# Performance work log

Measured on AMD Instinct MI355X. Metric: run time of the kernel, lower is better.

The kernel has to match this reference:

```python
import jax, jax.numpy as jnp
import numpy as np

N = 50000      # total atoms in batched graph
E = 800000     # edges
IN = 128       # in_feats
OUT = 64       # out_feats (per GAT head)
H = 4          # num_heads
NEG_SLOPE = 0.2
BN_EPS = 1e-5


def setup_inputs() -> dict:
    key = jax.random.key(0)
    ks = jax.random.split(key, 16)
    s = 0.1  # keep activations well-scaled
    return {
        "node_feats": jax.random.normal(ks[0], (N, IN), jnp.float32),
        "W_fc":       jax.random.normal(ks[1], (IN, H * OUT), jnp.float32) * s,
        "attn_l":     jax.random.normal(ks[2], (H, OUT), jnp.float32) * s,
        "attn_r":     jax.random.normal(ks[3], (H, OUT), jnp.float32) * s,
        "gat_res_w":  jax.random.normal(ks[4], (IN, H * OUT), jnp.float32) * s,
        "gat_bias":   jax.random.normal(ks[5], (H * OUT,), jnp.float32) * s,
        "conv_w":     jax.random.normal(ks[6], (1, H, 1), jnp.float32) * s,
        "conv_b":     jax.random.normal(ks[7], (1,), jnp.float32) * s,
        "res_w":      jax.random.normal(ks[8], (IN, OUT), jnp.float32) * s,
        "res_b":      jax.random.normal(ks[9], (OUT,), jnp.float32) * s,
        "bn_gamma":   jnp.ones((OUT,), jnp.float32),
        "bn_beta":    jnp.zeros((OUT,), jnp.float32),
        "src":        jax.random.randint(ks[10], (E,), 0, N, jnp.int32),
        "dst":        jax.random.randint(ks[11], (E,), 0, N, jnp.int32),
        "etype":      0,
    }


def reference(node_feats, W_fc, attn_l, attn_r, gat_res_w, gat_bias,
              conv_w, conv_b, res_w, res_b, bn_gamma, bn_beta,
              src, dst, etype):
    # ---- GATConv (DGL semantics, eval mode: no dropout) ----
    h = (node_feats @ W_fc).reshape(-1, H, OUT)            # [N,H,D]
    el = jnp.sum(h * attn_l, axis=-1)                      # [N,H]
    er = jnp.sum(h * attn_r, axis=-1)                      # [N,H]
    e = jax.nn.leaky_relu(el[src] + er[dst], NEG_SLOPE)    # [E,H]
    # segment softmax over incoming edges of each dst node
    m = jax.ops.segment_max(e, dst, num_segments=N)        # [N,H]
    m = jnp.where(jnp.isfinite(m), m, 0.0)                 # empty segments
    a = jnp.exp(e - m[dst])                                # [E,H]
    ssum = jax.ops.segment_sum(a, dst, num_segments=N)     # [N,H]
    alpha = a / (ssum[dst] + 1e-16)                        # [E,H]
    # weighted aggregation: rst[v] = sum_{(u->v)} alpha * h[u]
    rst = jax.ops.segment_sum(alpha[:, :, None] * h[src], dst, num_segments=N)  # [N,H,D]
    # GAT residual (in != H*OUT -> linear res_fc, no bias) + bias + activation
    rst = rst + (node_feats @ gat_res_w).reshape(-1, H, OUT) + gat_bias.reshape(H, OUT)
    rst = jax.nn.relu(rst)                                 # [N,H,D]
    # ---- Conv1d(4 -> 1, kernel=1): weighted head merge ----
    y = jnp.einsum("nhd,h->nd", rst, conv_w[0, :, 0]) + conv_b[0]  # [N,D]
    # ---- outer residual ----
    y = y + jax.nn.relu(node_feats @ res_w + res_b)
    # ---- BatchNorm1d (training-style batch stats) ----
    mean = jnp.mean(y, axis=0)
    var = jnp.var(y, axis=0)
    return (y - mean) / jnp.sqrt(var + BN_EPS) * bn_gamma + bn_beta
```

## Files before the change

### kernel.cpp

```cpp
#include <hip/hip_runtime.h>

#define IN_F   128
#define OUTD   64
#define HOUT   256
#define RESTC  320
#define NEG_SLOPE 0.2f
#define BN_EPS 1e-5f
#define HIST_BLOCKS 512
#define BPAD 136

typedef __attribute__((ext_vector_type(8))) short bf16x8;
typedef __attribute__((ext_vector_type(4))) float f32x4;
typedef __attribute__((ext_vector_type(2))) float f32x2;

__device__ __forceinline__ unsigned short f2bf(float f) {
    union { float f; unsigned u; } v; v.f = f;
    unsigned r = (v.u + 0x7FFF + ((v.u >> 16) & 1)) >> 16;
    return (unsigned short)r;
}
__device__ __forceinline__ float bf2f(unsigned short h) {
    union { unsigned u; float f; } v; v.u = ((unsigned)h) << 16;
    return v.f;
}

__global__ __launch_bounds__(256) void k0_pack(
    const float* __restrict__ W_fc, const float* __restrict__ W_gres,
    const float* __restrict__ W_res, unsigned short* __restrict__ Btg)
{
    int idx = blockIdx.x * 256 + threadIdx.x;
    if (idx >= 576 * 128) return;
    int c = idx >> 7, k = idx & 127;
    float v;
    if (c < 256)      v = W_fc[k * HOUT + c];
    else if (c < 512) v = W_gres[k * HOUT + (c - 256)];
    else              v = W_res[k * OUTD + (c - 512)];
    Btg[idx] = f2bf(v);
}

__global__ __launch_bounds__(256) void k1_gemm(
    const float* __restrict__ A, const unsigned short* __restrict__ Btg,
    const float* __restrict__ attn_l, const float* __restrict__ attn_r,
    const int* __restrict__ dst, int* __restrict__ degree, int* __restrict__ rank,
    unsigned char* __restrict__ Hh8, unsigned short* __restrict__ Hrest,
    float* __restrict__ el, float* __restrict__ er,
    int N, int E, int Mtiles)
{
    __shared__ __align__(16) unsigned short As[128 * BPAD];
    __shared__ __align__(16) unsigned short Bs[64 * BPAD];
    int bid = blockIdx.x, t = threadIdx.x;

    if (bid >= Mtiles) {
        int hb = bid - Mtiles;
        for (int e = hb * 256 + t; e < E; e += HIST_BLOCKS * 256)
            rank[e] = atomicAdd(degree + dst[e], 1);
        return;
    }

    int m0 = bid * 128;

    for (int i = 0; i < 16; ++i) {
        int slot = t + i * 256;
        int r = slot >> 5, c4 = (slot & 31) << 2;
        float4 v = make_float4(0.f, 0.f, 0.f, 0.f);
        if (m0 + r < N) v = *(const float4*)(A + (size_t)(m0 + r) * IN_F + c4);
        ushort4 o;
        o.x = f2bf(v.x); o.y = f2bf(v.y); o.z = f2bf(v.z); o.w = f2bf(v.w);
        *(ushort4*)(&As[r * BPAD + c4]) = o;
    }

    int w = t >> 6, lane = t & 63, quad = lane >> 4, n15 = lane & 15;
    bf16x8 af[2][4];
    unsigned hpack[2][4][4] = {};

    for (int n = 0; n < 9; ++n) {
        if (n) __syncthreads();
        for (int i = 0; i < 4; ++i) {
            int slot = t + i * 256;
            int c = slot >> 4, k0 = (slot & 15) << 3;
            *(uint4*)(&Bs[c * BPAD + k0]) = *(const uint4*)(Btg + (size_t)(n * 64 + c) * IN_F + k0);
        }
        __syncthreads();
        if (n == 0) {
#pragma unroll
            for (int i = 0; i < 2; ++i)
#pragma unroll
                for (int ks = 0; ks < 4; ++ks)
                    af[i][ks] = *(const bf16x8*)(&As[(w * 32 + i * 16 + n15) * BPAD + ks * 32 + quad * 8]);
        }

        f32x4 acc[2][4] = {};
#pragma unroll
        for (int ks = 0; ks < 4; ++ks) {
            bf16x8 bfr[4];
#pragma unroll
            for (int j = 0; j < 4; ++j)
                bfr[j] = *(const bf16x8*)(&Bs[(j * 16 + n15) * BPAD + ks * 32 + quad * 8]);
#pragma unroll
            for (int i = 0; i < 2; ++i)
#pragma unroll
                for (int j = 0; j < 4; ++j)
                    acc[i][j] = __builtin_amdgcn_mfma_f32_16x16x32_bf16(af[i][ks], bfr[j], acc[i][j], 0, 0, 0);
        }

        if (n < 4) {
            float alv[4], arv[4];
#pragma unroll
            for (int j = 0; j < 4; ++j) {
                alv[j] = attn_l[n * 64 + j * 16 + n15];
                arv[j] = attn_r[n * 64 + j * 16 + n15];
            }
#pragma unroll
            for (int i = 0; i < 2; ++i)
#pragma unroll
                for (int reg = 0; reg < 4; ++reg) {
                    float pl = acc[i][0][reg] * alv[0] + acc[i][1][reg] * alv[1]
                             + acc[i][2][reg] * alv[2] + acc[i][3][reg] * alv[3];
                    float pr = acc[i][0][reg] * arv[0] + acc[i][1][reg] * arv[1]
                             + acc[i][2][reg] * arv[2] + acc[i][3][reg] * arv[3];
#pragma unroll
                    for (int off = 1; off < 16; off <<= 1) {
                        pl += __shfl_xor(pl, off);
                        pr += __shfl_xor(pr, off);
                    }
                    int r = m0 + w * 32 + i * 16 + quad * 4 + reg;
                    if (n15 == 0 && r < N) {
                        el[(size_t)r * 4 + n] = pl;
                        er[(size_t)r * 4 + n] = pr;
                    }
                }
#pragma unroll
            for (int i = 0; i < 2; ++i)
#pragma unroll
                for (int j = 0; j < 4; ++j)
#pragma unroll
                    for (int reg = 0; reg < 4; ++reg) {
                        float v = acc[i][j][reg];
                        unsigned pk = (unsigned)__builtin_amdgcn_cvt_pk_fp8_f32(v, v, 0, false);
                        hpack[i][j][reg] |= (pk & 0xffu) << (8 * n);
                    }
        } else {
            int c0 = (n - 4) * 64;
#pragma unroll
            for (int i = 0; i < 2; ++i) {
                int rbase = m0 + w * 32 + i * 16 + quad * 4;
#pragma unroll
                for (int reg = 0; reg < 4; ++reg) {
                    int r = rbase + reg;
                    if (r < N) {
#pragma unroll
                        for (int j = 0; j < 4; ++j)
                            Hrest[(size_t)r * RESTC + c0 + j * 16 + n15] = f2bf(acc[i][j][reg]);
                    }
                }
            }
        }
    }

#pragma unroll
    for (int i = 0; i < 2; ++i) {
        int rbase = m0 + w * 32 + i * 16 + quad * 4;
#pragma unroll
        for (int reg = 0; reg < 4; ++reg) {
            int r = rbase + reg;
            if (r < N) {
#pragma unroll
                for (int j = 0; j < 4; ++j)
                    *(unsigned*)(Hh8 + (size_t)r * 256 + (j * 16 + n15) * 4) = hpack[i][j][reg];
            }
        }
    }
}

__global__ __launch_bounds__(256) void scanA_kernel(const int* __restrict__ degree,
                                                    int* __restrict__ excl,
                                                    int* __restrict__ blocksum, int N) {
    __shared__ int sm[256];
    int t = threadIdx.x;
    int i = blockIdx.x * 256 + t;
    int d = (i < N) ? degree[i] : 0;
    sm[t] = d; __syncthreads();
    for (int off = 1; off < 256; off <<= 1) {
        int v = (t >= off) ? sm[t - off] : 0;
        __syncthreads();
        sm[t] += v;
        __syncthreads();
    }
    if (i < N) excl[i] = sm[t] - d;
    if (t == 255) blocksum[blockIdx.x] = sm[255];
}

__global__ __launch_bounds__(256) void scanB_kernel(const int* __restrict__ blocksum,
                                                    int* __restrict__ base, int nb) {
    __shared__ int sm[256];
    int t = threadIdx.x;
    int d = (t < nb) ? blocksum[t] : 0;
    sm[t] = d; __syncthreads();
    for (int off = 1; off < 256; off <<= 1) {
        int v = (t >= off) ? sm[t - off] : 0;
        __syncthreads();
        sm[t] += v;
        __syncthreads();
    }
    if (t < nb) base[t] = sm[t] - d;
}

__global__ void scatter_kernel(const int* __restrict__ src, const int* __restrict__ dst,
                               const int* __restrict__ rank, const int* __restrict__ excl,
                               const int* __restrict__ base,
                               const float* __restrict__ el, const float* __restrict__ er,
                               uint4* __restrict__ es_sorted, int E) {
    int e = blockIdx.x * 256 + threadIdx.x;
    if (e >= E) return;
    int d = dst[e], u = src[e];
    int p = excl[d] + base[d >> 8] + rank[e];
    float4 l = *(const float4*)(el + (size_t)u * 4);
    float4 r = *(const float4*)(er + (size_t)d * 4);
    float x, s0, s1, s2, s3;
    x = l.x + r.x; x = x > 0.f ? x : NEG_SLOPE * x; s0 = __expf(x);
    x = l.y + r.y; x = x > 0.f ? x : NEG_SLOPE * x; s1 = __expf(x);
    x = l.z + r.z; x = x > 0.f ? x : NEG_SLOPE * x; s2 = __expf(x);
    x = l.w + r.w; x = x > 0.f ? x : NEG_SLOPE * x; s3 = __expf(x);
    uint4 o;
    o.x = (unsigned)u;
    o.y = (unsigned)f2bf(s0) | ((unsigned)f2bf(s1) << 16);
    o.z = (unsigned)f2bf(s2) | ((unsigned)f2bf(s3) << 16);
    o.w = 0u;
    es_sorted[p] = o;
}

__global__ __launch_bounds__(256) void agg_kernel(
    const unsigned char* __restrict__ Hh8, const unsigned short* __restrict__ Hrest,
    const int* __restrict__ excl, const int* __restrict__ base,
    const uint4* __restrict__ es_sorted,
    const float* __restrict__ gat_bias, const float* __restrict__ conv_w,
    const float* __restrict__ conv_b, const float* __restrict__ res_b,
    float* __restrict__ y, int N, int E)
{
    int wave = threadIdx.x >> 6, lane = threadIdx.x & 63;
    int v = blockIdx.x * 4 + wave;
    if (v >= N) return;
    int b  = excl[v] + base[v >> 8];
    int e2 = (v + 1 < N) ? (excl[v + 1] + base[(v + 1) >> 8]) : E;
    int deg = e2 - b;

    float a0 = 0.f, a1 = 0.f, a2 = 0.f, a3 = 0.f;
    float p0 = 0.f, p1 = 0.f, p2 = 0.f, p3 = 0.f;

    for (int i0 = 0; i0 < deg; i0 += 64) {
        int j = i0 + lane;
        uint4 es = make_uint4(0u, 0u, 0u, 0u);
        if (j < deg) es = es_sorted[b + j];
        p0 += bf2f((unsigned short)(es.y & 0xffff));
        p1 += bf2f((unsigned short)(es.y >> 16));
        p2 += bf2f((unsigned short)(es.z & 0xffff));
        p3 += bf2f((unsigned short)(es.z >> 16));
        int cl = deg - i0; if (cl > 64) cl = 64;
        for (int jj = 0; jj < cl; ++jj) {
            unsigned uu  = __shfl(es.x, jj);
            unsigned s01 = __shfl(es.y, jj);
            unsigned s23 = __shfl(es.z, jj);
            unsigned hv = *(const unsigned*)(Hh8 + (size_t)uu * 256 + lane * 4);
            f32x2 lo = __builtin_amdgcn_cvt_pk_f32_fp8(hv, false);
            f32x2 hi = __builtin_amdgcn_cvt_pk_f32_fp8(hv, true);
            a0 += bf2f((unsigned short)(s01 & 0xffff)) * lo.x;
            a1 += bf2f((unsigned short)(s01 >> 16))    * lo.y;
            a2 += bf2f((unsigned short)(s23 & 0xffff)) * hi.x;
            a3 += bf2f((unsigned short)(s23 >> 16))    * hi.y;
        }
    }
#pragma unroll
    for (int off = 1; off < 64; off <<= 1) {
        p0 += __shfl_xor(p0, off); p1 += __shfl_xor(p1, off);
        p2 += __shfl_xor(p2, off); p3 += __shfl_xor(p3, off);
    }
    float r0 = 1.f / (p0 + 1e-16f), r1 = 1.f / (p1 + 1e-16f);
    float r2 = 1.f / (p2 + 1e-16f), r3 = 1.f / (p3 + 1e-16f);

    const unsigned short* hr = Hrest + (size_t)v * RESTC;
    float yv = conv_b[0];
    float tt;
    tt = a0 * r0 + bf2f(hr[lane])       + gat_bias[lane];       tt = tt > 0.f ? tt : 0.f; yv += conv_w[0] * tt;
    tt = a1 * r1 + bf2f(hr[64 + lane])  + gat_bias[64 + lane];  tt = tt > 0.f ? tt : 0.f; yv += conv_w[1] * tt;
    tt = a2 * r2 + bf2f(hr[128 + lane]) + gat_bias[128 + lane]; tt = tt > 0.f ? tt : 0.f; yv += conv_w[2] * tt;
    tt = a3 * r3 + bf2f(hr[192 + lane]) + gat_bias[192 + lane]; tt = tt > 0.f ? tt : 0.f; yv += conv_w[3] * tt;
    float resv = bf2f(hr[256 + lane]) + res_b[lane];
    yv += resv > 0.f ? resv : 0.f;
    y[(size_t)v * OUTD + lane] = yv;
}

__global__ __launch_bounds__(256) void bn_partial_kernel(const float* __restrict__ y,
                                                         float* __restrict__ bnsum,
                                                         float* __restrict__ bnsumsq, int total) {
    __shared__ float smem[256];
    int t = threadIdx.x;
    size_t idx = (size_t)blockIdx.x * 256 + t;
    size_t stride = (size_t)gridDim.x * 256;
    float sum = 0.f, sq = 0.f;
    for (; idx < (size_t)total; idx += stride) {
        float v = y[idx];
        sum += v; sq += v * v;
    }
    int d = t & 63;
    smem[t] = sum; __syncthreads();
    if (t < 64) atomicAdd(bnsum + d, smem[t] + smem[t + 64] + smem[t + 128] + smem[t + 192]);
    __syncthreads();
    smem[t] = sq; __syncthreads();
    if (t < 64) atomicAdd(bnsumsq + d, smem[t] + smem[t + 64] + smem[t + 128] + smem[t + 192]);
}

__global__ void norm_kernel(const float* __restrict__ y,
                            const float* __restrict__ bnsum, const float* __restrict__ bnsumsq,
                            const float* __restrict__ gamma, const float* __restrict__ beta,
                            float* __restrict__ out, int total4, float invN) {
    int idx = blockIdx.x * blockDim.x + threadIdx.x;
    if (idx >= total4) return;
    float4 v = *(const float4*)(y + (size_t)idx * 4);
    int d = (idx * 4) & 63;
    float4 o;
#pragma unroll
    for (int k = 0; k < 4; ++k) {
        float mean = bnsum[d + k] * invN;
        float var = bnsumsq[d + k] * invN - mean * mean;
        float sc = gamma[d + k] * rsqrtf(var + BN_EPS);
        float sh = beta[d + k] - mean * sc;
        float val = (&v.x)[k] * sc + sh;
        (&o.x)[k] = val;
    }
    *(float4*)(out + (size_t)idx * 4) = o;
}

extern "C" void kernel_launch(void* const* d_in, const int* in_sizes, int n_in,
                              void* d_out, int out_size, void* d_ws, size_t ws_size,
                              hipStream_t stream) {
    const float* node_feats = (const float*)d_in[0];
    const float* W_fc       = (const float*)d_in[1];
    const float* attn_l     = (const float*)d_in[2];
    const float* attn_r     = (const float*)d_in[3];
    const float* gat_res_w  = (const float*)d_in[4];
    const float* gat_bias   = (const float*)d_in[5];
    const float* conv_w     = (const float*)d_in[6];
    const float* conv_b     = (const float*)d_in[7];
    const float* res_w      = (const float*)d_in[8];
    const float* res_b      = (const float*)d_in[9];
    const float* bn_gamma   = (const float*)d_in[10];
    const float* bn_beta    = (const float*)d_in[11];
    const int*   src        = (const int*)d_in[12];
    const int*   dst        = (const int*)d_in[13];

    const int N = in_sizes[0] / IN_F;
    const int E = in_sizes[12];
    const int Mtiles = (N + 127) / 128;
    const int nb = (N + 255) / 256;

    char* ws = (char*)d_ws;
    size_t off = 0;
    auto alloc = [&](size_t bytes) -> void* {
        void* p = (void*)(ws + off);
        off += (bytes + 255) & ~(size_t)255;
        return p;
    };

    int*   degree  = (int*)alloc((size_t)N * 4);
    float* bnsum   = (float*)alloc(64 * 4);
    float* bnsumsq = (float*)alloc(64 * 4);
    size_t zero_bytes = off;
    int*            rank      = (int*)alloc((size_t)E * 4);
    int*            excl      = (int*)alloc((size_t)N * 4);
    int*            blocksum  = (int*)alloc(256 * 4);
    int*            base      = (int*)alloc(256 * 4);
    uint4*          es_sorted = (uint4*)alloc((size_t)E * 16);
    unsigned short* Btg       = (unsigned short*)alloc((size_t)576 * IN_F * 2);
    unsigned char*  Hh8       = (unsigned char*)alloc((size_t)N * 256);
    unsigned short* Hrest     = (unsigned short*)alloc((size_t)N * RESTC * 2);
    float*          el        = (float*)alloc((size_t)N * 4 * 4);
    float*          er        = (float*)alloc((size_t)N * 4 * 4);
    float*          y         = (float*)alloc((size_t)N * OUTD * 4);
    (void)ws_size; (void)n_in; (void)out_size;

    hipMemsetAsync(d_ws, 0, zero_bytes, stream);

    k0_pack<<<(576 * 128 + 255) / 256, 256, 0, stream>>>(W_fc, gat_res_w, res_w, Btg);
    k1_gemm<<<Mtiles + HIST_BLOCKS, 256, 0, stream>>>(node_feats, Btg, attn_l, attn_r,
                                                      dst, degree, rank, Hh8, Hrest,
                                                      el, er, N, E, Mtiles);
    scanA_kernel<<<nb, 256, 0, stream>>>(degree, excl, blocksum, N);
    scanB_kernel<<<1, 256, 0, stream>>>(blocksum, base, nb);
    scatter_kernel<<<(E + 255) / 256, 256, 0, stream>>>(src, dst, rank, excl, base,
                                                        el, er, es_sorted, E);
    agg_kernel<<<(N + 3) / 4, 256, 0, stream>>>(Hh8, Hrest, excl, base, es_sorted,
                                                gat_bias, conv_w, conv_b, res_b, y, N, E);
    bn_partial_kernel<<<512, 256, 0, stream>>>(y, bnsum, bnsumsq, N * OUTD);
    norm_kernel<<<(N * OUTD / 4 + 255) / 256, 256, 0, stream>>>(y, bnsum, bnsumsq,
                                                                bn_gamma, bn_beta, (float*)d_out,
                                                                N * OUTD / 4, 1.f / (float)N);
}
```

Measured before the change: 268.5 us.

## Store GAT residual in fp8 with folded biases, shrink GEMM tile, unroll aggregation

The GAT residual projection is now written as interleaved fp8 (Hr8) with gat_bias folded in, and the outer residual as bf16 with res_b folded in. This replaces the wide bf16 Hrest buffer, cutting GEMM write traffic and agg read traffic. The GEMM M-tile drops from 128 to 64 rows, giving more blocks and lower register use. The agg inner loop uses readlane with a 2-way unroll and a pre-shifted source offset. fp8 residuals add quantization error.

```diff
diff --git a/kernel.cpp b/kernel.cpp
--- a/kernel.cpp
+++ b/kernel.cpp
@@ -3,7 +3,6 @@
 #define IN_F   128
 #define OUTD   64
 #define HOUT   256
-#define RESTC  320
 #define NEG_SLOPE 0.2f
 #define BN_EPS 1e-5f
 #define HIST_BLOCKS 512
@@ -40,12 +39,14 @@
 __global__ __launch_bounds__(256) void k1_gemm(
     const float* __restrict__ A, const unsigned short* __restrict__ Btg,
     const float* __restrict__ attn_l, const float* __restrict__ attn_r,
+    const float* __restrict__ gat_bias, const float* __restrict__ res_b,
     const int* __restrict__ dst, int* __restrict__ degree, int* __restrict__ rank,
-    unsigned char* __restrict__ Hh8, unsigned short* __restrict__ Hrest,
+    unsigned char* __restrict__ Hh8, unsigned char* __restrict__ Hr8,
+    unsigned short* __restrict__ Rres,
     float* __restrict__ el, float* __restrict__ er,
     int N, int E, int Mtiles)
 {
-    __shared__ __align__(16) unsigned short As[128 * BPAD];
+    __shared__ __align__(16) unsigned short As[64 * BPAD];
     __shared__ __align__(16) unsigned short Bs[64 * BPAD];
     int bid = blockIdx.x, t = threadIdx.x;
 
@@ -56,9 +57,9 @@
         return;
     }
 
-    int m0 = bid * 128;
-
-    for (int i = 0; i < 16; ++i) {
+    int m0 = bid * 64;
+
+    for (int i = 0; i < 8; ++i) {
         int slot = t + i * 256;
         int r = slot >> 5, c4 = (slot & 31) << 2;
         float4 v = make_float4(0.f, 0.f, 0.f, 0.f);
@@ -69,8 +70,9 @@
     }
 
     int w = t >> 6, lane = t & 63, quad = lane >> 4, n15 = lane & 15;
-    bf16x8 af[2][4];
-    unsigned hpack[2][4][4] = {};
+    bf16x8 af[4];
+    unsigned hpack[4][4] = {};
+    unsigned rpack[4][4] = {};
 
     for (int n = 0; n < 9; ++n) {
         if (n) __syncthreads();
@@ -82,13 +84,11 @@
         __syncthreads();
         if (n == 0) {
 #pragma unroll
-            for (int i = 0; i < 2; ++i)
-#pragma unroll
-                for (int ks = 0; ks < 4; ++ks)
-                    af[i][ks] = *(const bf16x8*)(&As[(w * 32 + i * 16 + n15) * BPAD + ks * 32 + quad * 8]);
-        }
-
-        f32x4 acc[2][4] = {};
+            for (int ks = 0; ks < 4; ++ks)
+                af[ks] = *(const bf16x8*)(&As[(w * 16 + n15) * BPAD + ks * 32 + quad * 8]);
+        }
+
+        f32x4 acc[4] = {};
 #pragma unroll
         for (int ks = 0; ks < 4; ++ks) {
             bf16x8 bfr[4];
@@ -96,10 +96,8 @@
             for (int j = 0; j < 4; ++j)
                 bfr[j] = *(const bf16x8*)(&Bs[(j * 16 + n15) * BPAD + ks * 32 + quad * 8]);
 #pragma unroll
-            for (int i = 0; i < 2; ++i)
-#pragma unroll
-                for (int j = 0; j < 4; ++j)
-                    acc[i][j] = __builtin_amdgcn_mfma_f32_16x16x32_bf16(af[i][ks], bfr[j], acc[i][j], 0, 0, 0);
+            for (int j = 0; j < 4; ++j)
+                acc[j] = __builtin_amdgcn_mfma_f32_16x16x32_bf16(af[ks], bfr[j], acc[j], 0, 0, 0);
         }
 
         if (n < 4) {
@@ -110,62 +108,67 @@
                 arv[j] = attn_r[n * 64 + j * 16 + n15];
             }
 #pragma unroll
-            for (int i = 0; i < 2; ++i)
-#pragma unroll
-                for (int reg = 0; reg < 4; ++reg) {
-                    float pl = acc[i][0][reg] * alv[0] + acc[i][1][reg] * alv[1]
-                             + acc[i][2][reg] * alv[2] + acc[i][3][reg] * alv[3];
-                    float pr = acc[i][0][reg] * arv[0] + acc[i][1][reg] * arv[1]
-                             + acc[i][2][reg] * arv[2] + acc[i][3][reg] * arv[3];
-#pragma unroll
-                    for (int off = 1; off < 16; off <<= 1) {
-                        pl += __shfl_xor(pl, off);
-                        pr += __shfl_xor(pr, off);
-                    }
-                    int r = m0 + w * 32 + i * 16 + quad * 4 + reg;
-                    if (n15 == 0 && r < N) {
-                        el[(size_t)r * 4 + n] = pl;
-                        er[(size_t)r * 4 + n] = pr;
-                    }
+            for (int reg = 0; reg < 4; ++reg) {
+                float pl = acc[0][reg] * alv[0] + acc[1][reg] * alv[1]
+                         + acc[2][reg] * alv[2] + acc[3][reg] * alv[3];
+                float pr = acc[0][reg] * arv[0] + acc[1][reg] * arv[1]
+                         + acc[2][reg] * arv[2] + acc[3][reg] * arv[3];
+#pragma unroll
+                for (int off = 1; off < 16; off <<= 1) {
+                    pl += __shfl_xor(pl, off);
+                    pr += __shfl_xor(pr, off);
                 }
-#pragma unroll
-            for (int i = 0; i < 2; ++i)
-#pragma unroll
-                for (int j = 0; j < 4; ++j)
-#pragma unroll
-                    for (int reg = 0; reg < 4; ++reg) {
-                        float v = acc[i][j][reg];
-                        unsigned pk = (unsigned)__builtin_amdgcn_cvt_pk_fp8_f32(v, v, 0, false);
-                        hpack[i][j][reg] |= (pk & 0xffu) << (8 * n);
-                    }
-        } else {
-            int c0 = (n - 4) * 64;
-#pragma unroll
-            for (int i = 0; i < 2; ++i) {
-                int rbase = m0 + w * 32 + i * 16 + quad * 4;
-#pragma unroll
-                for (int reg = 0; reg < 4; ++reg) {
-                    int r = rbase + reg;
-                    if (r < N) {
-#pragma unroll
-                        for (int j = 0; j < 4; ++j)
-                            Hrest[(size_t)r * RESTC + c0 + j * 16 + n15] = f2bf(acc[i][j][reg]);
-                    }
+                int r = m0 + w * 16 + quad * 4 + reg;
+                if (n15 == 0 && r < N) {
+                    el[(size_t)r * 4 + n] = pl;
+                    er[(size_t)r * 4 + n] = pr;
                 }
             }
-        }
-    }
-
-#pragma unroll
-    for (int i = 0; i < 2; ++i) {
-        int rbase = m0 + w * 32 + i * 16 + quad * 4;
-#pragma unroll
-        for (int reg = 0; reg < 4; ++reg) {
-            int r = rbase + reg;
-            if (r < N) {
-#pragma unroll
-                for (int j = 0; j < 4; ++j)
-                    *(unsigned*)(Hh8 + (size_t)r * 256 + (j * 16 + n15) * 4) = hpack[i][j][reg];
+#pragma unroll
+            for (int j = 0; j < 4; ++j)
+#pragma unroll
+                for (int reg = 0; reg < 4; ++reg) {
+                    float v = acc[j][reg];
+                    unsigned pk = (unsigned)__builtin_amdgcn_cvt_pk_fp8_f32(v, v, 0, false);
+                    hpack[j][reg] |= (pk & 0xffu) << (8 * n);
+                }
+        } else if (n < 8) {
+            int hd = n - 4;
+            float bv[4];
+#pragma unroll
+            for (int j = 0; j < 4; ++j) bv[j] = gat_bias[hd * 64 + j * 16 + n15];
+#pragma unroll
+            for (int j = 0; j < 4; ++j)
+#pragma unroll
+                for (int reg = 0; reg < 4; ++reg) {
+                    float v = acc[j][reg] + bv[j];
+                    unsigned pk = (unsigned)__builtin_amdgcn_cvt_pk_fp8_f32(v, v, 0, false);
+                    rpack[j][reg] |= (pk & 0xffu) << (8 * hd);
+                }
+        } else {
+            float bv[4];
+#pragma unroll
+            for (int j = 0; j < 4; ++j) bv[j] = res_b[j * 16 + n15];
+#pragma unroll
+            for (int reg = 0; reg < 4; ++reg) {
+                int r = m0 + w * 16 + quad * 4 + reg;
+                if (r < N) {
+#pragma unroll
+                    for (int j = 0; j < 4; ++j)
+                        Rres[(size_t)r * OUTD + j * 16 + n15] = f2bf(acc[j][reg] + bv[j]);
+                }
+            }
+        }
+    }
+
+#pragma unroll
+    for (int reg = 0; reg < 4; ++reg) {
+        int r = m0 + w * 16 + quad * 4 + reg;
+        if (r < N) {
+#pragma unroll
+            for (int j = 0; j < 4; ++j) {
+                *(unsigned*)(Hh8 + ((size_t)r << 8) + (j * 16 + n15) * 4) = hpack[j][reg];
+                *(unsigned*)(Hr8 + ((size_t)r << 8) + (j * 16 + n15) * 4) = rpack[j][reg];
             }
         }
     }
@@ -221,7 +224,7 @@
     x = l.z + r.z; x = x > 0.f ? x : NEG_SLOPE * x; s2 = __expf(x);
     x = l.w + r.w; x = x > 0.f ? x : NEG_SLOPE * x; s3 = __expf(x);
     uint4 o;
-    o.x = (unsigned)u;
+    o.x = (unsigned)u << 8;
     o.y = (unsigned)f2bf(s0) | ((unsigned)f2bf(s1) << 16);
     o.z = (unsigned)f2bf(s2) | ((unsigned)f2bf(s3) << 16);
     o.w = 0u;
@@ -229,11 +232,11 @@
 }
 
 __global__ __launch_bounds__(256) void agg_kernel(
-    const unsigned char* __restrict__ Hh8, const unsigned short* __restrict__ Hrest,
+    const unsigned char* __restrict__ Hh8, const unsigned char* __restrict__ Hr8,
+    const unsigned short* __restrict__ Rres,
     const int* __restrict__ excl, const int* __restrict__ base,
     const uint4* __restrict__ es_sorted,
-    const float* __restrict__ gat_bias, const float* __restrict__ conv_w,
-    const float* __restrict__ conv_b, const float* __restrict__ res_b,
+    const float* __restrict__ conv_w, const float* __restrict__ conv_b,
     float* __restrict__ y, int N, int E)
 {
     int wave = threadIdx.x >> 6, lane = threadIdx.x & 63;
@@ -243,6 +246,7 @@
     int e2 = (v + 1 < N) ? (excl[v + 1] + base[(v + 1) >> 8]) : E;
     int deg = e2 - b;
 
+    const unsigned char* hbase = Hh8 + lane * 4;
     float a0 = 0.f, a1 = 0.f, a2 = 0.f, a3 = 0.f;
     float p0 = 0.f, p1 = 0.f, p2 = 0.f, p3 = 0.f;
 
@@ -255,17 +259,40 @@
         p2 += bf2f((unsigned short)(es.z & 0xffff));
         p3 += bf2f((unsigned short)(es.z >> 16));
         int cl = deg - i0; if (cl > 64) cl = 64;
-        for (int jj = 0; jj < cl; ++jj) {
-            unsigned uu  = __shfl(es.x, jj);
-            unsigned s01 = __shfl(es.y, jj);
-            unsigned s23 = __shfl(es.z, jj);
-            unsigned hv = *(const unsigned*)(Hh8 + (size_t)uu * 256 + lane * 4);
-            f32x2 lo = __builtin_amdgcn_cvt_pk_f32_fp8(hv, false);
-            f32x2 hi = __builtin_amdgcn_cvt_pk_f32_fp8(hv, true);
-            a0 += bf2f((unsigned short)(s01 & 0xffff)) * lo.x;
-            a1 += bf2f((unsigned short)(s01 >> 16))    * lo.y;
-            a2 += bf2f((unsigned short)(s23 & 0xffff)) * hi.x;
-            a3 += bf2f((unsigned short)(s23 >> 16))    * hi.y;
+        int jj = 0;
+        for (; jj + 1 < cl; jj += 2) {
+            unsigned uA   = (unsigned)__builtin_amdgcn_readlane((int)es.x, jj);
+            unsigned sA01 = (unsigned)__builtin_amdgcn_readlane((int)es.y, jj);
+            unsigned sA23 = (unsigned)__builtin_amdgcn_readlane((int)es.z, jj);
+            unsigned uB   = (unsigned)__builtin_amdgcn_readlane((int)es.x, jj + 1);
+            unsigned sB01 = (unsigned)__builtin_amdgcn_readlane((int)es.y, jj + 1);
+            unsigned sB23 = (unsigned)__builtin_amdgcn_readlane((int)es.z, jj + 1);
+            unsigned hvA = *(const unsigned*)(hbase + uA);
+            unsigned hvB = *(const unsigned*)(hbase + uB);
+            f32x2 loA = __builtin_amdgcn_cvt_pk_f32_fp8(hvA, false);
+            f32x2 hiA = __builtin_amdgcn_cvt_pk_f32_fp8(hvA, true);
+            f32x2 loB = __builtin_amdgcn_cvt_pk_f32_fp8(hvB, false);
+            f32x2 hiB = __builtin_amdgcn_cvt_pk_f32_fp8(hvB, true);
+            a0 += bf2f((unsigned short)(sA01 & 0xffff)) * loA.x;
+            a1 += bf2f((unsigned short)(sA01 >> 16))    * loA.y;
+            a2 += bf2f((unsigned short)(sA23 & 0xffff)) * hiA.x;
+            a3 += bf2f((unsigned short)(sA23 >> 16))    * hiA.y;
+            a0 += bf2f((unsigned short)(sB01 & 0xffff)) * loB.x;
+            a1 += bf2f((unsigned short)(sB01 >> 16))    * loB.y;
+            a2 += bf2f((unsigned short)(sB23 & 0xffff)) * hiB.x;
+            a3 += bf2f((unsigned short)(sB23 >> 16))    * hiB.y;
+        }
+        if (jj < cl) {
+            unsigned uA   = (unsigned)__builtin_amdgcn_readlane((int)es.x, jj);
+            unsigned sA01 = (unsigned)__builtin_amdgcn_readlane((int)es.y, jj);
+            unsigned sA23 = (unsigned)__builtin_amdgcn_readlane((int)es.z, jj);
+            unsigned hvA = *(const unsigned*)(hbase + uA);
+            f32x2 loA = __builtin_amdgcn_cvt_pk_f32_fp8(hvA, false);
+            f32x2 hiA = __builtin_amdgcn_cvt_pk_f32_fp8(hvA, true);
+            a0 += bf2f((unsigned short)(sA01 & 0xffff)) * loA.x;
+            a1 += bf2f((unsigned short)(sA01 >> 16))    * loA.y;
+            a2 += bf2f((unsigned short)(sA23 & 0xffff)) * hiA.x;
+            a3 += bf2f((unsigned short)(sA23 >> 16))    * hiA.y;
         }
     }
 #pragma unroll
@@ -276,15 +303,16 @@
     float r0 = 1.f / (p0 + 1e-16f), r1 = 1.f / (p1 + 1e-16f);
     float r2 = 1.f / (p2 + 1e-16f), r3 = 1.f / (p3 + 1e-16f);
 
-    const unsigned short* hr = Hrest + (size_t)v * RESTC;
-    float yv = conv_b[0];
+    unsigned hr = *(const unsigned*)(Hr8 + ((size_t)v << 8) + lane * 4);
+    f32x2 rlo = __builtin_amdgcn_cvt_pk_f32_fp8(hr, false);
+    f32x2 rhi = __builtin_amdgcn_cvt_pk_f32_fp8(hr, true);
+    float resv = bf2f(Rres[(size_t)v * OUTD + lane]);
+    float yv = conv_b[0] + (resv > 0.f ? resv : 0.f);
     float tt;
-    tt = a0 * r0 + bf2f(hr[lane])       + gat_bias[lane];       tt = tt > 0.f ? tt : 0.f; yv += conv_w[0] * tt;
-    tt = a1 * r1 + bf2f(hr[64 + lane])  + gat_bias[64 + lane];  tt = tt > 0.f ? tt : 0.f; yv += conv_w[1] * tt;
-    tt = a2 * r2 + bf2f(hr[128 + lane]) + gat_bias[128 + lane]; tt = tt > 0.f ? tt : 0.f; yv += conv_w[2] * tt;
-    tt = a3 * r3 + bf2f(hr[192 + lane]) + gat_bias[192 + lane]; tt = tt > 0.f ? tt : 0.f; yv += conv_w[3] * tt;
-    float resv = bf2f(hr[256 + lane]) + res_b[lane];
-    yv += resv > 0.f ? resv : 0.f;
+    tt = a0 * r0 + rlo.x; tt = tt > 0.f ? tt : 0.f; yv += conv_w[0] * tt;
+    tt = a1 * r1 + rlo.y; tt = tt > 0.f ? tt : 0.f; yv += conv_w[1] * tt;
+    tt = a2 * r2 + rhi.x; tt = tt > 0.f ? tt : 0.f; yv += conv_w[2] * tt;
+    tt = a3 * r3 + rhi.y; tt = tt > 0.f ? tt : 0.f; yv += conv_w[3] * tt;
     y[(size_t)v * OUTD + lane] = yv;
 }
 
@@ -323,8 +351,7 @@
         float var = bnsumsq[d + k] * invN - mean * mean;
         float sc = gamma[d + k] * rsqrtf(var + BN_EPS);
         float sh = beta[d + k] - mean * sc;
-        float val = (&v.x)[k] * sc + sh;
-        (&o.x)[k] = val;
+        (&o.x)[k] = (&v.x)[k] * sc + sh;
     }
     *(float4*)(out + (size_t)idx * 4) = o;
 }
@@ -349,7 +376,7 @@
 
     const int N = in_sizes[0] / IN_F;
     const int E = in_sizes[12];
-    const int Mtiles = (N + 127) / 128;
+    const int Mtiles = (N + 63) / 64;
     const int nb = (N + 255) / 256;
 
     char* ws = (char*)d_ws;
@@ -371,7 +398,8 @@
     uint4*          es_sorted = (uint4*)alloc((size_t)E * 16);
     unsigned short* Btg       = (unsigned short*)alloc((size_t)576 * IN_F * 2);
     unsigned char*  Hh8       = (unsigned char*)alloc((size_t)N * 256);
-    unsigned short* Hrest     = (unsigned short*)alloc((size_t)N * RESTC * 2);
+    unsigned char*  Hr8       = (unsigned char*)alloc((size_t)N * 256);
+    unsigned short* Rres      = (unsigned short*)alloc((size_t)N * OUTD * 2);
     float*          el        = (float*)alloc((size_t)N * 4 * 4);
     float*          er        = (float*)alloc((size_t)N * 4 * 4);
     float*          y         = (float*)alloc((size_t)N * OUTD * 4);
@@ -381,14 +409,14 @@
 
     k0_pack<<<(576 * 128 + 255) / 256, 256, 0, stream>>>(W_fc, gat_res_w, res_w, Btg);
     k1_gemm<<<Mtiles + HIST_BLOCKS, 256, 0, stream>>>(node_feats, Btg, attn_l, attn_r,
-                                                      dst, degree, rank, Hh8, Hrest,
-                                                      el, er, N, E, Mtiles);
+                                                      gat_bias, res_b, dst, degree, rank,
+                                                      Hh8, Hr8, Rres, el, er, N, E, Mtiles);
     scanA_kernel<<<nb, 256, 0, stream>>>(degree, excl, blocksum, N);
     scanB_kernel<<<1, 256, 0, stream>>>(blocksum, base, nb);
     scatter_kernel<<<(E + 255) / 256, 256, 0, stream>>>(src, dst, rank, excl, base,
                                                         el, er, es_sorted, E);
-    agg_kernel<<<(N + 3) / 4, 256, 0, stream>>>(Hh8, Hrest, excl, base, es_sorted,
-                                                gat_bias, conv_w, conv_b, res_b, y, N, E);
+    agg_kernel<<<(N + 3) / 4, 256, 0, stream>>>(Hh8, Hr8, Rres, excl, base, es_sorted,
+                                                conv_w, conv_b, y, N, E);
     bn_partial_kernel<<<512, 256, 0, stream>>>(y, bnsum, bnsumsq, N * OUTD);
     norm_kernel<<<(N * OUTD / 4 + 255) / 256, 256, 0, stream>>>(y, bnsum, bnsumsq,
                                                                 bn_gamma, bn_beta, (float*)d_out,
```

Measured after the change: 271.2 us. No clear change (+1.0%).
